# Kernel optimization log

Measured on AMD Instinct MI355X. Metric: run time of the kernel, lower is better.

## Reference

```python
import jax, jax.numpy as jnp
import numpy as np

N_NODES, N_EDGES, N_TRIP = 100000, 200000, 600000
HID, HEADS, RADIUS = 256, 8, 3
ATOM_F, BOND_F = 133, 14

def setup_inputs() -> dict:
    key = jax.random.key(0)
    ks = jax.random.split(key, 20)
    def w(k, i, o):
        return jax.random.normal(k, (i, o), dtype=jnp.float32) / np.sqrt(i)
    L = RADIUS - 1
    return {
        'atom_feature': jax.random.normal(ks[0], (N_NODES, ATOM_F), dtype=jnp.float32),
        'edge_feature': jax.random.normal(ks[1], (N_EDGES, BOND_F), dtype=jnp.float32),
        'W_i': w(ks[2], ATOM_F + BOND_F, HID),
        'Wq': jnp.stack([w(jax.random.fold_in(ks[3], l), HID, HID) for l in range(L)]),
        'Wk': jnp.stack([w(jax.random.fold_in(ks[4], l), HID, HID) for l in range(L)]),
        'Wv': jnp.stack([w(jax.random.fold_in(ks[5], l), HID, HID) for l in range(L)]),
        'L1w': jnp.stack([w(jax.random.fold_in(ks[6], l), HID, HID) for l in range(L)]),
        'L1b': jnp.zeros((L, HID), dtype=jnp.float32),
        'L2w': jnp.stack([w(jax.random.fold_in(ks[7], l), HID, HID) for l in range(L)]),
        'L2b': jnp.zeros((L, HID), dtype=jnp.float32),
        'Wo': w(ks[8], ATOM_F + HID, HID),
        'bo': jnp.zeros((HID,), dtype=jnp.float32),
        'src': jax.random.randint(ks[9], (N_EDGES,), 0, N_NODES, dtype=jnp.int32),
        'dst': jax.random.randint(ks[10], (N_EDGES,), 0, N_NODES, dtype=jnp.int32),
        'idx_kj': jax.random.randint(ks[11], (N_TRIP,), 0, N_EDGES, dtype=jnp.int32),
        'idx_ji': jax.random.randint(ks[12], (N_TRIP,), 0, N_EDGES, dtype=jnp.int32),
    }

def _att_layer(feats, Wq, Wk, Wv, l1w, l1b, l2w, l2b, idx_kj, idx_ji):
    E = feats.shape[0]
    d = HID // HEADS
    q = (feats @ Wq).reshape(E, HEADS, d)
    k = (feats @ Wk).reshape(E, HEADS, d)
    v = (feats @ Wv).reshape(E, HEADS, d)
    # per-triplet attention logits [T, heads, 1]
    att = jnp.sum(q[idx_kj] * k[idx_ji], axis=-1, keepdims=True)
    att = jnp.exp(jax.nn.leaky_relu(att, negative_slope=0.2))
    denom = jax.ops.segment_sum(att, idx_ji, num_segments=E)  # edge softmax norm
    att = att / denom[idx_ji]
    v_att = (v[idx_kj] * att).reshape(-1, HID)
    v_flat = v.reshape(E, HID)
    # v_clone = v + index_add(v_att) - v == segment_sum of messages
    v_clone = jax.ops.segment_sum(v_att, idx_ji, num_segments=E)
    # residual MLP (dropout p=0 -> identity)
    h = jax.nn.relu(jax.nn.relu(v_clone @ l1w + l1b) @ l2w + l2b)
    return v_flat + h

def reference(atom_feature, edge_feature, W_i, Wq, Wk, Wv, L1w, L1b, L2w, L2b, Wo, bo, src, dst, idx_kj, idx_ji):
    # per-edge initial feature: concat(src atom feature, edge feature)
    init = jnp.concatenate([atom_feature[src], edge_feature], axis=1)
    feats = jax.nn.relu(init @ W_i)
    for l in range(RADIUS - 1):
        feats = _att_layer(feats, Wq[l], Wk[l], Wv[l], L1w[l], L1b[l], L2w[l], L2b[l], idx_kj, idx_ji)
    # edge -> node sum (dgl update_all copy_e + sum onto dst)
    feats_sum = jax.ops.segment_sum(feats, dst, num_segments=atom_feature.shape[0])
    a_input = jnp.concatenate([atom_feature, feats_sum], axis=1)
    return jax.nn.relu(a_input @ Wo + bo)
```

## Files before the change

kernel.cpp:

```cpp
#include <hip/hip_runtime.h>
#include <stdint.h>

#define NN 100000
#define NNP 100096
#define NE 200000
#define NEP 200064
#define NT 600000
#define HID 256

typedef __attribute__((ext_vector_type(8))) short bf16x8;
typedef __attribute__((ext_vector_type(4))) float f32x4;

__device__ __forceinline__ float bf2f(unsigned short u) {
    union { unsigned int i; float f; } x; x.i = ((unsigned int)u) << 16; return x.f;
}
__device__ __forceinline__ unsigned short f2bf(float f) {
    union { float f; unsigned int i; } x; x.f = f;
    unsigned int r = (x.i + 0x7FFFu + ((x.i >> 16) & 1u)) >> 16;
    return (unsigned short)r;
}

__device__ __forceinline__ void gload16(const void* g, void* l) {
    __builtin_amdgcn_global_load_lds(
        (const __attribute__((address_space(1))) void*)g,
        (__attribute__((address_space(3))) void*)l, 16, 0, 0);
}

template<int FLAGS, bool CBF>
__device__ __forceinline__
void gemm128_core(const unsigned short* __restrict__ A,
                  const unsigned short* __restrict__ BT,
                  const float* __restrict__ bias,
                  const unsigned short* __restrict__ res,
                  void* __restrict__ Cv, int row0, int col0,
                  int Mreal, int Kpad,
                  unsigned short* Asb, unsigned short* Bsb)
{
    const int t    = threadIdx.x;
    const int lane = t & 63;
    const int wv   = t >> 6;
    const int wr   = wv >> 1;
    const int wc   = wv & 1;
    const int l15  = lane & 15;
    const int lk   = lane >> 4;
    const int sub  = lane >> 3;
    const int schk = lane & 7;

    f32x4 acc[4][4];
#pragma unroll
    for (int i = 0; i < 4; ++i)
#pragma unroll
        for (int j = 0; j < 4; ++j) acc[i][j] = (f32x4){0.f, 0.f, 0.f, 0.f};

    const int nt = Kpad >> 6;
    for (int kt = 0; kt < nt; ++kt) {
        const int k0 = kt << 6;
#pragma unroll
        for (int j = 0; j < 4; ++j) {
            const int ii = wv * 4 + j;
            const int r  = ii * 8 + sub;
            const int cg = schk ^ (r & 7);
            gload16(A + (size_t)(row0 + r) * Kpad + k0 + cg * 8, Asb + ii * 512);
        }
#pragma unroll
        for (int j = 0; j < 4; ++j) {
            const int ii = wv * 4 + j;
            const int r  = ii * 8 + sub;
            const int cg = schk ^ (r & 7);
            gload16(BT + (size_t)(col0 + r) * Kpad + k0 + cg * 8, Bsb + ii * 512);
        }
        __syncthreads();
#pragma unroll
        for (int ks = 0; ks < 2; ++ks) {
            bf16x8 af[4], bfg[4];
#pragma unroll
            for (int mi = 0; mi < 4; ++mi) {
                const int r = wr * 64 + mi * 16 + l15;
                const int c = ks * 4 + lk;
                af[mi] = *(const bf16x8*)((const char*)Asb
                          + r * 128 + ((c ^ (r & 7)) << 4));
            }
#pragma unroll
            for (int ni = 0; ni < 4; ++ni) {
                const int r = wc * 64 + ni * 16 + l15;
                const int c = ks * 4 + lk;
                bfg[ni] = *(const bf16x8*)((const char*)Bsb
                           + r * 128 + ((c ^ (r & 7)) << 4));
            }
#pragma unroll
            for (int mi = 0; mi < 4; ++mi)
#pragma unroll
                for (int ni = 0; ni < 4; ++ni)
                    acc[mi][ni] = __builtin_amdgcn_mfma_f32_16x16x32_bf16(
                        af[mi], bfg[ni], acc[mi][ni], 0, 0, 0);
        }
        __syncthreads();
    }

#pragma unroll
    for (int mi = 0; mi < 4; ++mi) {
#pragma unroll
        for (int r = 0; r < 4; ++r) {
            const int row = row0 + wr * 64 + mi * 16 + lk * 4 + r;
            if (row >= Mreal) continue;
#pragma unroll
            for (int ni = 0; ni < 4; ++ni) {
                const int col = col0 + wc * 64 + ni * 16 + l15;
                float o = acc[mi][ni][r];
                if (FLAGS & 2) o += bias[col];
                if (FLAGS & 1) o = fmaxf(o, 0.f);
                if (FLAGS & 4) o += bf2f(res[(size_t)row * HID + col]);
                if (CBF) ((unsigned short*)Cv)[(size_t)row * HID + col] = f2bf(o);
                else     ((float*)Cv)[(size_t)row * HID + col] = o;
            }
        }
    }
}

template<int FLAGS, bool CBF>
__global__ __launch_bounds__(256, 3)
void gemm128(const unsigned short* __restrict__ A,
             const unsigned short* __restrict__ BT,
             const float* __restrict__ bias,
             const unsigned short* __restrict__ res,
             void* __restrict__ Cv, int Mtiles, int Mreal, int Kpad)
{
    __shared__ alignas(16) unsigned short Asb[128 * 64];
    __shared__ alignas(16) unsigned short Bsb[128 * 64];
    const int x   = blockIdx.x;
    const int xcd = x & 7;
    const int ii  = x >> 3;
    const int g   = (ii >> 1) * 8 + xcd;
    const int ch  = ii & 1;
    if (g >= Mtiles) return;
    gemm128_core<FLAGS, CBF>(A, BT, bias, res, Cv, g * 128, ch * 128,
                             Mreal, Kpad, Asb, Bsb);
}

__global__ __launch_bounds__(256, 3)
void gemm128_qkv(const unsigned short* __restrict__ A,
                 const unsigned short* __restrict__ BTq,
                 const unsigned short* __restrict__ BTk,
                 const unsigned short* __restrict__ BTv,
                 unsigned short* __restrict__ Cq,
                 unsigned short* __restrict__ Ck,
                 unsigned short* __restrict__ Cvp, int Mtiles)
{
    __shared__ alignas(16) unsigned short Asb[128 * 64];
    __shared__ alignas(16) unsigned short Bsb[128 * 64];
    const int x   = blockIdx.x;
    const int xcd = x & 7;
    const int ii  = x >> 3;
    const int g   = (ii / 6) * 8 + xcd;
    const int j   = ii % 6;
    if (g >= Mtiles) return;
    const int proj = j >> 1;
    const int ch   = j & 1;
    const unsigned short* BT = (proj == 0) ? BTq : (proj == 1) ? BTk : BTv;
    unsigned short*       C  = (proj == 0) ? Cq  : (proj == 1) ? Ck  : Cvp;
    gemm128_core<0, true>(A, BT, nullptr, nullptr, C, g * 128, ch * 128,
                          NE, 256, Asb, Bsb);
}

__global__ __launch_bounds__(256)
void wconv(const float* __restrict__ W, unsigned short* __restrict__ BT,
           int Kreal, int Kpad)
{
    const int idx = blockIdx.x * 256 + threadIdx.x;
    const int n = idx / Kpad, kp = idx - n * Kpad;
    float v = (kp < Kreal) ? W[(size_t)kp * HID + n] : 0.f;
    BT[idx] = f2bf(v);
}

__global__ __launch_bounds__(256)
void wconv10(const float* __restrict__ Wq, const float* __restrict__ Wk,
             const float* __restrict__ Wv, const float* __restrict__ L1w,
             const float* __restrict__ L2w, unsigned short* __restrict__ outbase)
{
    const int y = blockIdx.y;
    const int l = y / 5, which = y - l * 5;
    const float* src;
    switch (which) {
        case 0: src = Wq;  break;
        case 1: src = Wk;  break;
        case 2: src = Wv;  break;
        case 3: src = L1w; break;
        default: src = L2w; break;
    }
    src += (size_t)l * 65536;
    const int idx = blockIdx.x * 256 + threadIdx.x;
    const int n = idx >> 8, kp = idx & 255;
    outbase[(size_t)y * 65536 + idx] = f2bf(src[(size_t)kp * HID + n]);
}

__global__ __launch_bounds__(256)
void build_initA(const float* __restrict__ atom, const float* __restrict__ edge,
                 const int* __restrict__ src, unsigned short* __restrict__ out)
{
    const long total = (long)NE * 192;
    long idx = (long)blockIdx.x * blockDim.x + threadIdx.x;
    if (idx >= total) return;
    const int e = (int)(idx / 192);
    const int c = (int)(idx - (long)e * 192);
    float v = 0.f;
    if (c < 133)      v = atom[(size_t)src[e] * 133 + c];
    else if (c < 147) v = edge[(size_t)e * 14 + (c - 133)];
    out[idx] = f2bf(v);
}

__global__ __launch_bounds__(256)
void build_finalA(const float* __restrict__ atom, const float* __restrict__ fsum,
                  unsigned short* __restrict__ out)
{
    const long total = (long)NNP * 448;
    long idx = (long)blockIdx.x * blockDim.x + threadIdx.x;
    if (idx >= total) return;
    const int n = (int)(idx / 448);
    const int c = (int)(idx - (long)n * 448);
    float v = 0.f;
    if (n < NN) {
        if (c < 133)      v = atom[(size_t)n * 133 + c];
        else if (c < 389) v = fsum[(size_t)n * 256 + (c - 133)];
    }
    out[idx] = f2bf(v);
}

__global__ __launch_bounds__(256)
void count_keys(const int* __restrict__ key, int n, int nkeys, int* __restrict__ cnt)
{
    const int i = blockIdx.x * 256 + threadIdx.x;
    if (i < n) {
        const int kk = key[i];
        if ((unsigned)kk < (unsigned)nkeys) atomicAdd(&cnt[kk], 1);
    }
}

__global__ __launch_bounds__(256)
void fill_lists(const int* __restrict__ key, int n, int nkeys, int cap,
                int* __restrict__ cur, int* __restrict__ list)
{
    const int i = blockIdx.x * 256 + threadIdx.x;
    if (i < n) {
        const int kk = key[i];
        if ((unsigned)kk >= (unsigned)nkeys) return;
        const int pos = atomicAdd(&cur[kk], 1);
        if ((unsigned)pos < (unsigned)cap) list[pos] = i;
    }
}

__global__ __launch_bounds__(256)
void scan1(const int* __restrict__ in, int n, int* __restrict__ excl,
           int* __restrict__ part)
{
    __shared__ int sh[256];
    const int t = threadIdx.x;
    const int base = blockIdx.x * 1024 + t * 4;
    int v[4]; int s = 0;
#pragma unroll
    for (int j = 0; j < 4; ++j) { v[j] = (base + j < n) ? in[base + j] : 0; s += v[j]; }
    sh[t] = s; __syncthreads();
    for (int off = 1; off < 256; off <<= 1) {
        int x = (t >= off) ? sh[t - off] : 0;
        __syncthreads();
        sh[t] += x;
        __syncthreads();
    }
    int ex = sh[t] - s;
#pragma unroll
    for (int j = 0; j < 4; ++j) { if (base + j < n) excl[base + j] = ex; ex += v[j]; }
    if (t == 255) part[blockIdx.x] = sh[255];
}

__global__ __launch_bounds__(256)
void scan2(int* __restrict__ part, int nparts)
{
    __shared__ int sh[256];
    const int t = threadIdx.x;
    const int v = (t < nparts) ? part[t] : 0;
    sh[t] = v; __syncthreads();
    for (int off = 1; off < 256; off <<= 1) {
        int x = (t >= off) ? sh[t - off] : 0;
        __syncthreads();
        sh[t] += x;
        __syncthreads();
    }
    if (t < nparts) part[t] = sh[t] - v;
}

__global__ __launch_bounds__(256)
void scan3(const int* __restrict__ excl, const int* __restrict__ part,
           const int* counts, int n, int* __restrict__ offs, int* cur)
{
    const int i = blockIdx.x * 256 + threadIdx.x;
    if (i >= n) return;
    const int v = excl[i] + part[i >> 10];
    const int c = counts[i];
    offs[i] = v;
    cur[i] = v;
    if (i == n - 1) offs[n] = v + c;
}

__global__ __launch_bounds__(256)
void gather_v(const unsigned short* __restrict__ q, const unsigned short* __restrict__ k,
              const unsigned short* __restrict__ v,
              const int* __restrict__ toff, const int* __restrict__ tlist,
              const int* __restrict__ idx_kj,
              unsigned short* __restrict__ vc)
{
    const long gtid = (long)blockIdx.x * blockDim.x + threadIdx.x;
    const int w    = (int)(gtid >> 5);
    const int lane = threadIdx.x & 31;
    if (w >= NE) return;
    int beg = toff[w], end = toff[w + 1];
    if (beg < 0) beg = 0;
    if (end > NT) end = NT;

    const bf16x8 kv = *(const bf16x8*)(k + (size_t)w * HID + lane * 8);
    float kf[8];
#pragma unroll
    for (int j = 0; j < 8; ++j) kf[j] = bf2f((unsigned short)kv[j]);

    float av[8];
#pragma unroll
    for (int j = 0; j < 8; ++j) av[j] = 0.f;
    float den = 0.f;

    int kj_next = -1;
    if (beg < end) {
        const int tt = tlist[beg];
        kj_next = ((unsigned)tt < (unsigned)NT) ? idx_kj[tt] : -1;
    }
    for (int p = beg; p < end; ++p) {
        const int kj = kj_next;
        if (p + 1 < end) {
            const int tt = tlist[p + 1];
            kj_next = ((unsigned)tt < (unsigned)NT) ? idx_kj[tt] : -1;
        }
        if ((unsigned)kj >= (unsigned)NE) continue;
        const bf16x8 qv = *(const bf16x8*)(q + (size_t)kj * HID + lane * 8);
        float s = 0.f;
#pragma unroll
        for (int j = 0; j < 8; ++j) s += bf2f((unsigned short)qv[j]) * kf[j];
        s += __shfl_xor(s, 1);
        s += __shfl_xor(s, 2);
        const float lr = (s > 0.f) ? s : 0.2f * s;
        const float a  = __expf(lr);
        den += a;
        const bf16x8 vv = *(const bf16x8*)(v + (size_t)kj * HID + lane * 8);
#pragma unroll
        for (int j = 0; j < 8; ++j) av[j] += a * bf2f((unsigned short)vv[j]);
    }
    const float inv = (den != 0.f) ? 1.f / den : 0.f;
    bf16x8 o;
#pragma unroll
    for (int j = 0; j < 8; ++j) o[j] = (short)f2bf(av[j] * inv);
    *(bf16x8*)(vc + (size_t)w * HID + lane * 8) = o;
}

__global__ __launch_bounds__(256)
void gather_node(const unsigned short* __restrict__ feats,
                 const int* __restrict__ noff, const int* __restrict__ nlist,
                 float* __restrict__ fsum)
{
    const int w    = (int)(((long)blockIdx.x * blockDim.x + threadIdx.x) >> 6);
    const int lane = threadIdx.x & 63;
    if (w >= NN) return;
    int beg = noff[w], end = noff[w + 1];
    if (beg < 0) beg = 0;
    if (end > NE) end = NE;
    float a0 = 0.f, a1 = 0.f, a2 = 0.f, a3 = 0.f;
    for (int p = beg; p < end; ++p) {
        const int e = nlist[p];
        if ((unsigned)e >= (unsigned)NE) continue;
        const ushort4 f = *(const ushort4*)(feats + (size_t)e * HID + lane * 4);
        a0 += bf2f(f.x); a1 += bf2f(f.y); a2 += bf2f(f.z); a3 += bf2f(f.w);
    }
    float4 o = make_float4(a0, a1, a2, a3);
    *(float4*)(fsum + (size_t)w * HID + lane * 4) = o;
}

extern "C" void kernel_launch(void* const* d_in, const int* in_sizes, int n_in,
                              void* d_out, int out_size, void* d_ws, size_t ws_size,
                              hipStream_t stream)
{
    const float* atom = (const float*)d_in[0];
    const float* edge = (const float*)d_in[1];
    const float* W_i  = (const float*)d_in[2];
    const float* Wq   = (const float*)d_in[3];
    const float* Wk   = (const float*)d_in[4];
    const float* Wv   = (const float*)d_in[5];
    const float* L1w  = (const float*)d_in[6];
    const float* L1b  = (const float*)d_in[7];
    const float* L2w  = (const float*)d_in[8];
    const float* L2b  = (const float*)d_in[9];
    const float* Wo   = (const float*)d_in[10];
    const float* bo   = (const float*)d_in[11];
    const int* src    = (const int*)d_in[12];
    const int* dst    = (const int*)d_in[13];
    const int* idx_kj = (const int*)d_in[14];
    const int* idx_ji = (const int*)d_in[15];

    const size_t RB = (size_t)NE * HID * 2;
    char* ws = (char*)d_ws;
    unsigned short* feats = (unsigned short*)(ws);
    unsigned short* qb    = (unsigned short*)(ws + RB);
    unsigned short* kb    = (unsigned short*)(ws + 2 * RB);
    unsigned short* vb    = (unsigned short*)d_out;
    unsigned short* vc    = feats;
    unsigned short* initA = qb;
    unsigned short* h1    = kb;
    float*          fsum  = (float*)(ws + RB);
    unsigned short* finalA = kb;

    char* p = ws + 3 * RB;
    int* trip_off  = (int*)p; p += 800016;
    int* trip_cur  = (int*)p; p += 800016;
    int* trip_list = (int*)p; p += 2400000;
    int* node_off  = (int*)p; p += 400016;
    int* node_cur  = (int*)p; p += 400016;
    int* node_list = (int*)p; p += 800000;
    int* tmp_excl  = (int*)p; p += 800016;
    int* partials  = (int*)p; p += 1024;
    unsigned short* wiT = (unsigned short*)p; p += (size_t)256 * 192 * 2;
    unsigned short* wT0 = (unsigned short*)p; p += (size_t)10 * 65536 * 2;
    unsigned short* woT = (unsigned short*)p; p += (size_t)256 * 448 * 2;
    const size_t NEEDED = (size_t)(p - ws);
    if (ws_size < NEEDED) return;
    auto wT = [&](int i) { return wT0 + (size_t)i * 65536; };

    const int MT_E  = NEP / 128;
    const int MT_E8 = ((MT_E + 7) / 8) * 8;
    const int MT_N  = NNP / 128;
    const int MT_N8 = ((MT_N + 7) / 8) * 8;

    wconv<<<192, 256, 0, stream>>>(W_i, wiT, 147, 192);
    wconv10<<<dim3(256, 10), 256, 0, stream>>>(Wq, Wk, Wv, L1w, L2w, wT0);
    wconv<<<448, 256, 0, stream>>>(Wo, woT, 389, 448);

    hipMemsetAsync(trip_cur, 0, (size_t)NE * 4, stream);
    hipMemsetAsync(node_cur, 0, (size_t)NN * 4, stream);
    count_keys<<<(NT + 255) / 256, 256, 0, stream>>>(idx_ji, NT, NE, trip_cur);
    count_keys<<<(NE + 255) / 256, 256, 0, stream>>>(dst, NE, NN, node_cur);

    scan1<<<(NE + 1023) / 1024, 256, 0, stream>>>(trip_cur, NE, tmp_excl, partials);
    scan2<<<1, 256, 0, stream>>>(partials, (NE + 1023) / 1024);
    scan3<<<(NE + 255) / 256, 256, 0, stream>>>(tmp_excl, partials, trip_cur, NE, trip_off, trip_cur);
    fill_lists<<<(NT + 255) / 256, 256, 0, stream>>>(idx_ji, NT, NE, NT, trip_cur, trip_list);

    scan1<<<(NN + 1023) / 1024, 256, 0, stream>>>(node_cur, NN, tmp_excl, partials);
    scan2<<<1, 256, 0, stream>>>(partials, (NN + 1023) / 1024);
    scan3<<<(NN + 255) / 256, 256, 0, stream>>>(tmp_excl, partials, node_cur, NN, node_off, node_cur);
    fill_lists<<<(NE + 255) / 256, 256, 0, stream>>>(dst, NE, NN, NE, node_cur, node_list);

    {
        const long total = (long)NE * 192;
        build_initA<<<(int)((total + 255) / 256), 256, 0, stream>>>(atom, edge, src, initA);
    }
    gemm128<1, true><<<MT_E8 * 2, 256, 0, stream>>>(initA, wiT, nullptr, nullptr,
                                                    feats, MT_E, NE, 192);

    for (int l = 0; l < 2; ++l) {
        const float* l1b = L1b + (size_t)l * 256;
        const float* l2b = L2b + (size_t)l * 256;

        gemm128_qkv<<<MT_E8 * 6, 256, 0, stream>>>(
            feats, wT(l * 5 + 0), wT(l * 5 + 1), wT(l * 5 + 2), qb, kb, vb, MT_E);

        gather_v<<<(NE * 32) / 256, 256, 0, stream>>>(qb, kb, vb, trip_off, trip_list, idx_kj, vc);

        gemm128<3, true><<<MT_E8 * 2, 256, 0, stream>>>(vc, wT(l * 5 + 3), l1b,
                                                        nullptr, h1, MT_E, NE, 256);
        gemm128<7, true><<<MT_E8 * 2, 256, 0, stream>>>(h1, wT(l * 5 + 4), l2b,
                                                        vb, feats, MT_E, NE, 256);
    }

    gather_node<<<NN / 4, 256, 0, stream>>>(feats, node_off, node_list, fsum);
    {
        const long total = (long)NNP * 448;
        build_finalA<<<(int)((total + 255) / 256), 256, 0, stream>>>(atom, fsum, finalA);
    }
    gemm128<3, false><<<MT_N8 * 2, 256, 0, stream>>>(finalA, woT, bo, nullptr,
                                                     d_out, MT_N, NN, 448);
}
```

Before: 1.340 ms.

## Widen GEMM tiles to 128x256 with 512-thread blocks covering full output width

The GEMM kernels move from 128x128 tiles on 256 threads to 128x256 tiles on 512 threads, so one block covers all 256 output columns. Each A row tile is now loaded once instead of twice, and the QKV launch uses one block per projection instead of two. The cost is a larger LDS footprint per block (48 KB) and fewer blocks. The plain GEMM also drops its XCD-aware block remapping. The launch bound of 512 threads with a minimum of 6 blocks may squeeze register allocation.

```diff
diff --git a/kernel.cpp b/kernel.cpp
--- a/kernel.cpp
+++ b/kernel.cpp
@@ -28,19 +28,18 @@
 
 template<int FLAGS, bool CBF>
 __device__ __forceinline__
-void gemm128_core(const unsigned short* __restrict__ A,
+void gemm256_core(const unsigned short* __restrict__ A,
                   const unsigned short* __restrict__ BT,
                   const float* __restrict__ bias,
                   const unsigned short* __restrict__ res,
-                  void* __restrict__ Cv, int row0, int col0,
-                  int Mreal, int Kpad,
+                  void* __restrict__ Cv, int row0, int Mreal, int Kpad,
                   unsigned short* Asb, unsigned short* Bsb)
 {
     const int t    = threadIdx.x;
     const int lane = t & 63;
-    const int wv   = t >> 6;
-    const int wr   = wv >> 1;
-    const int wc   = wv & 1;
+    const int wid  = t >> 6;
+    const int wr   = wid >> 2;
+    const int wc   = wid & 3;
     const int l15  = lane & 15;
     const int lk   = lane >> 4;
     const int sub  = lane >> 3;
@@ -56,18 +55,18 @@
     for (int kt = 0; kt < nt; ++kt) {
         const int k0 = kt << 6;
 #pragma unroll
-        for (int j = 0; j < 4; ++j) {
-            const int ii = wv * 4 + j;
+        for (int j = 0; j < 2; ++j) {
+            const int ii = wid * 2 + j;
             const int r  = ii * 8 + sub;
             const int cg = schk ^ (r & 7);
             gload16(A + (size_t)(row0 + r) * Kpad + k0 + cg * 8, Asb + ii * 512);
         }
 #pragma unroll
         for (int j = 0; j < 4; ++j) {
-            const int ii = wv * 4 + j;
+            const int ii = wid * 4 + j;
             const int r  = ii * 8 + sub;
             const int cg = schk ^ (r & 7);
-            gload16(BT + (size_t)(col0 + r) * Kpad + k0 + cg * 8, Bsb + ii * 512);
+            gload16(BT + (size_t)r * Kpad + k0 + cg * 8, Bsb + ii * 512);
         }
         __syncthreads();
 #pragma unroll
@@ -105,7 +104,7 @@
             if (row >= Mreal) continue;
 #pragma unroll
             for (int ni = 0; ni < 4; ++ni) {
-                const int col = col0 + wc * 64 + ni * 16 + l15;
+                const int col = wc * 64 + ni * 16 + l15;
                 float o = acc[mi][ni][r];
                 if (FLAGS & 2) o += bias[col];
                 if (FLAGS & 1) o = fmaxf(o, 0.f);
@@ -118,27 +117,23 @@
 }
 
 template<int FLAGS, bool CBF>
-__global__ __launch_bounds__(256, 3)
-void gemm128(const unsigned short* __restrict__ A,
+__global__ __launch_bounds__(512, 6)
+void gemm256(const unsigned short* __restrict__ A,
              const unsigned short* __restrict__ BT,
              const float* __restrict__ bias,
              const unsigned short* __restrict__ res,
              void* __restrict__ Cv, int Mtiles, int Mreal, int Kpad)
 {
     __shared__ alignas(16) unsigned short Asb[128 * 64];
-    __shared__ alignas(16) unsigned short Bsb[128 * 64];
-    const int x   = blockIdx.x;
-    const int xcd = x & 7;
-    const int ii  = x >> 3;
-    const int g   = (ii >> 1) * 8 + xcd;
-    const int ch  = ii & 1;
+    __shared__ alignas(16) unsigned short Bsb[256 * 64];
+    const int g = blockIdx.x;
     if (g >= Mtiles) return;
-    gemm128_core<FLAGS, CBF>(A, BT, bias, res, Cv, g * 128, ch * 128,
-                             Mreal, Kpad, Asb, Bsb);
-}
-
-__global__ __launch_bounds__(256, 3)
-void gemm128_qkv(const unsigned short* __restrict__ A,
+    gemm256_core<FLAGS, CBF>(A, BT, bias, res, Cv, g * 128, Mreal, Kpad,
+                             Asb, Bsb);
+}
+
+__global__ __launch_bounds__(512, 6)
+void gemm256_qkv(const unsigned short* __restrict__ A,
                  const unsigned short* __restrict__ BTq,
                  const unsigned short* __restrict__ BTk,
                  const unsigned short* __restrict__ BTv,
@@ -147,19 +142,17 @@
                  unsigned short* __restrict__ Cvp, int Mtiles)
 {
     __shared__ alignas(16) unsigned short Asb[128 * 64];
-    __shared__ alignas(16) unsigned short Bsb[128 * 64];
-    const int x   = blockIdx.x;
-    const int xcd = x & 7;
-    const int ii  = x >> 3;
-    const int g   = (ii / 6) * 8 + xcd;
-    const int j   = ii % 6;
+    __shared__ alignas(16) unsigned short Bsb[256 * 64];
+    const int x    = blockIdx.x;
+    const int xcd  = x & 7;
+    const int ii   = x >> 3;
+    const int g    = (ii / 3) * 8 + xcd;
+    const int proj = ii % 3;
     if (g >= Mtiles) return;
-    const int proj = j >> 1;
-    const int ch   = j & 1;
     const unsigned short* BT = (proj == 0) ? BTq : (proj == 1) ? BTk : BTv;
     unsigned short*       C  = (proj == 0) ? Cq  : (proj == 1) ? Ck  : Cvp;
-    gemm128_core<0, true>(A, BT, nullptr, nullptr, C, g * 128, ch * 128,
-                          NE, 256, Asb, Bsb);
+    gemm256_core<0, true>(A, BT, nullptr, nullptr, C, g * 128, NE, 256,
+                          Asb, Bsb);
 }
 
 __global__ __launch_bounds__(256)
@@ -456,22 +449,22 @@
         const long total = (long)NE * 192;
         build_initA<<<(int)((total + 255) / 256), 256, 0, stream>>>(atom, edge, src, initA);
     }
-    gemm128<1, true><<<MT_E8 * 2, 256, 0, stream>>>(initA, wiT, nullptr, nullptr,
-                                                    feats, MT_E, NE, 192);
+    gemm256<1, true><<<MT_E8, 512, 0, stream>>>(initA, wiT, nullptr, nullptr,
+                                                feats, MT_E, NE, 192);
 
     for (int l = 0; l < 2; ++l) {
         const float* l1b = L1b + (size_t)l * 256;
         const float* l2b = L2b + (size_t)l * 256;
 
-        gemm128_qkv<<<MT_E8 * 6, 256, 0, stream>>>(
+        gemm256_qkv<<<MT_E8 * 3, 512, 0, stream>>>(
             feats, wT(l * 5 + 0), wT(l * 5 + 1), wT(l * 5 + 2), qb, kb, vb, MT_E);
 
         gather_v<<<(NE * 32) / 256, 256, 0, stream>>>(qb, kb, vb, trip_off, trip_list, idx_kj, vc);
 
-        gemm128<3, true><<<MT_E8 * 2, 256, 0, stream>>>(vc, wT(l * 5 + 3), l1b,
-                                                        nullptr, h1, MT_E, NE, 256);
-        gemm128<7, true><<<MT_E8 * 2, 256, 0, stream>>>(h1, wT(l * 5 + 4), l2b,
-                                                        vb, feats, MT_E, NE, 256);
+        gemm256<3, true><<<MT_E8, 512, 0, stream>>>(vc, wT(l * 5 + 3), l1b,
+                                                    nullptr, h1, MT_E, NE, 256);
+        gemm256<7, true><<<MT_E8, 512, 0, stream>>>(h1, wT(l * 5 + 4), l2b,
+                                                    vb, feats, MT_E, NE, 256);
     }
 
     gather_node<<<NN / 4, 256, 0, stream>>>(feats, node_off, node_list, fsum);
@@ -479,6 +472,6 @@
         const long total = (long)NNP * 448;
         build_finalA<<<(int)((total + 255) / 256), 256, 0, stream>>>(atom, fsum, finalA);
     }
-    gemm128<3, false><<<MT_N8 * 2, 256, 0, stream>>>(finalA, woT, bo, nullptr,
-                                                     d_out, MT_N, NN, 448);
-}
+    gemm256<3, false><<<MT_N8, 512, 0, stream>>>(finalA, woT, bo, nullptr,
+                                                 d_out, MT_N, NN, 448);
+}
```

Measured after the change: 3.901 ms. +191.0%, slower.
